# Kernel optimization log

Hardware: AMD Instinct MI355X
Metric: run time of the kernel (lower is better)

Reference implementation:

```python
import jax, jax.numpy as jnp
import numpy as np

B, T, E, H, R = 1, 2048, 4096, 16, 64
D = E // H
SCALE_ATTN = float(np.sqrt(D))


def _i8_linear(x, W, b, alpha, beta):
    # W8A8B8O8Linear: int8 in, int8 weight/bias, int8 out with requant epilogue
    acc = jnp.einsum('bte,oe->bto', x.astype(jnp.int32), W.astype(jnp.int32)).astype(jnp.float32)
    y = alpha * acc + beta * b.astype(jnp.float32)
    return jnp.clip(jnp.round(y), -128, 127).astype(jnp.int8)


def _rotate_every_two(x):
    x1, x2 = x[..., ::2], x[..., 1::2]
    return jnp.stack([-x2, x1], axis=-1).reshape(x.shape)


def _sincos(seq_len, dim):
    inv_freq = 1.0 / (10000.0 ** (jnp.arange(0, dim, 2, dtype=jnp.float32) / dim))
    ang = jnp.arange(seq_len, dtype=jnp.float32)[:, None] * inv_freq[None, :]
    return jnp.sin(ang), jnp.cos(ang)


def _apply_rotary(x, sin, cos):
    # duplicate_interleave -> repeat each freq twice along last dim
    sin = jnp.repeat(sin, 2, axis=-1)[None, :, None, :]
    cos = jnp.repeat(cos, 2, axis=-1)[None, :, None, :]
    return x * cos + _rotate_every_two(x) * sin


def setup_inputs():
    key = jax.random.key(0)
    ks = jax.random.split(key, 9)
    i8 = lambda k, s: jax.random.randint(k, s, -128, 128, dtype=jnp.int32).astype(jnp.int8)
    return {
        'hidden_states': i8(ks[0], (B, T, E)),
        'Wq': i8(ks[1], (E, E)), 'bq': i8(ks[2], (E,)),
        'Wk': i8(ks[3], (E, E)), 'bk': i8(ks[4], (E,)),
        'Wv': i8(ks[5], (E, E)), 'bv': i8(ks[6], (E,)),
        'Wo': i8(ks[7], (E, E)),
        'b_out': jax.random.normal(ks[8], (E,), dtype=jnp.float32),
        'alpha_q': 2e-4, 'beta_q': 1.0,
        'alpha_k': 2e-4, 'beta_k': 1.0,
        'alpha_v': 2e-4, 'beta_v': 1.0,
        'alpha_qk': 1e-3, 'alpha_pv': 1e-2, 'alpha_out': 2e-4,
    }


def reference(hidden_states, Wq, bq, Wk, bk, Wv, bv, Wo, b_out,
              alpha_q, beta_q, alpha_k, beta_k, alpha_v, beta_v,
              alpha_qk, alpha_pv, alpha_out):
    # int8 q/k/v projections -> [B, T, H, D]
    q = _i8_linear(hidden_states, Wq, bq, alpha_q, beta_q).reshape(B, T, H, D)
    k = _i8_linear(hidden_states, Wk, bk, alpha_k, beta_k).reshape(B, T, H, D)
    v = _i8_linear(hidden_states, Wv, bv, alpha_v, beta_v).reshape(B, T, H, D)
    v = v.transpose(0, 2, 1, 3)  # [B, H, T, D] int8

    # fused rotary on first R dims (float math on dequantized-per-tensor int8 codes)
    sin, cos = _sincos(T, R)
    qf, kf = q.astype(jnp.float32), k.astype(jnp.float32)
    qf = jnp.concatenate([_apply_rotary(qf[..., :R], sin, cos), qf[..., R:]], axis=-1)
    kf = jnp.concatenate([_apply_rotary(kf[..., :R], sin, cos), kf[..., R:]], axis=-1)
    # torch .to(int8) truncates toward zero
    to_i8 = lambda x: jnp.clip(jnp.trunc(x), -128, 127).astype(jnp.int8)
    q = to_i8(qf.transpose(0, 2, 1, 3))  # [B, H, T, D]
    k = to_i8(kf.transpose(0, 2, 1, 3))

    scores = alpha_qk * jnp.einsum('bhtd,bhsd->bhts', q.astype(jnp.int32), k.astype(jnp.int32)).astype(jnp.float32)
    causal = jnp.tril(jnp.ones((T, T), dtype=bool))
    scores = jnp.where(causal, scores, jnp.finfo(jnp.float32).min)
    probs = jax.nn.softmax(scores / SCALE_ATTN, axis=-1)
    probs = jnp.round(probs * 127.0).astype(jnp.int8)  # requant probs to int8

    acc = jnp.einsum('bhts,bhsd->bhtd', probs.astype(jnp.int32), v.astype(jnp.int32)).astype(jnp.float32)
    attn_out = jnp.clip(jnp.round(alpha_pv * acc), -128, 127).astype(jnp.int8)
    attn_out = attn_out.transpose(0, 2, 1, 3).reshape(B, T, E)  # merge heads

    # W8A8BFP32OFP32Linear
    out = alpha_out * jnp.einsum('bte,oe->bto', attn_out.astype(jnp.int32), Wo.astype(jnp.int32)).astype(jnp.float32) + b_out
    return out
```

## Files before the change

### kernel.cpp

```cpp
#include <hip/hip_runtime.h>
#include <cstdint>
#include <cmath>

#define T_ 2048
#define E_ 4096
#define H_ 16
#define D_ 256
#define NF 32

typedef int v4i  __attribute__((ext_vector_type(4)));

__device__ __forceinline__ int dot4(int a, int b, int c) {
#if __has_builtin(__builtin_amdgcn_sdot4)
  return __builtin_amdgcn_sdot4(a, b, c, false);
#else
  c += ((a << 24) >> 24) * ((b << 24) >> 24);
  c += ((a << 16) >> 24) * ((b << 16) >> 24);
  c += ((a <<  8) >> 24) * ((b <<  8) >> 24);
  c += (a >> 24) * (b >> 24);
  return c;
#endif
}

__device__ __forceinline__ int pack4i(int4 v) {
  return (v.x & 255) | ((v.y & 255) << 8) | ((v.z & 255) << 16) | (v.w << 24);
}

#define GLD_LDS16(g, l)                                                        \
  __builtin_amdgcn_global_load_lds(                                            \
      (const __attribute__((address_space(1))) void*)(g),                      \
      (__attribute__((address_space(3))) void*)(l), 16, 0, 0)

__global__ void sincos_kernel(float* __restrict__ sinT, float* __restrict__ cosT) {
  int idx = blockIdx.x * 256 + threadIdx.x;
  int t = idx >> 5, j = idx & 31;
  float invf = (float)exp(-(double)j * (log(10000.0) / 32.0));
  float ang = (float)t * invf;
  sinT[idx] = (float)sin((double)ang);
  cosT[idx] = (float)cos((double)ang);
}

__global__ __launch_bounds__(256) void repack_kernel(const int* __restrict__ src,
                                                     int8_t* __restrict__ dst) {
  size_t i = (size_t)blockIdx.x * 256 + threadIdx.x;
  const int4* s = (const int4*)src + i * 4;
  int4 a = s[0], b = s[1], c = s[2], d = s[3];
  int4 o;
  o.x = pack4i(a); o.y = pack4i(b); o.z = pack4i(c); o.w = pack4i(d);
  ((int4*)dst)[i] = o;
}

__global__ __launch_bounds__(256, 3) void qkv_gemm_mfma(
    const int8_t* __restrict__ x8,
    const int8_t* __restrict__ Wq8, const int* __restrict__ bq,
    const int8_t* __restrict__ Wk8, const int* __restrict__ bk,
    const int8_t* __restrict__ Wv8, const int* __restrict__ bv,
    const float* __restrict__ alpq, const float* __restrict__ betq,
    const float* __restrict__ alpk, const float* __restrict__ betk,
    const float* __restrict__ alpv, const float* __restrict__ betv,
    int8_t* __restrict__ Q8, int8_t* __restrict__ K8, int8_t* __restrict__ VT)
{
  const int mode = blockIdx.z;
  const int8_t* __restrict__ W = (mode == 0) ? Wq8 : (mode == 1 ? Wk8 : Wv8);
  const int* __restrict__ bs   = (mode == 0) ? bq  : (mode == 1 ? bk  : bv);
  const float alpha = (mode == 0) ? alpq[0] : (mode == 1 ? alpk[0] : alpv[0]);
  const float beta  = (mode == 0) ? betq[0] : (mode == 1 ? betk[0] : betv[0]);

  __shared__ int8_t As[3][8192];
  __shared__ int8_t Bs[3][8192];

  const int tid  = threadIdx.x;
  const int wave = tid >> 6, lane = tid & 63;
  const int wm = wave >> 1, wn = wave & 1;
  const int t0 = blockIdx.x * 128, o0 = blockIdx.y * 128;

  const int srow = lane >> 2;
  const int scol = ((lane & 3) ^ ((lane >> 3) & 3)) * 16;
  const int col  = lane & 15;
  const int quad = lane >> 4;

  v4i acc[4][4] = {};

  const int8_t* gA0 = x8 + (size_t)(t0 + wave * 32 + srow) * E_ + scol;
  const int8_t* gB0 = W  + (size_t)(o0 + wave * 32 + srow) * E_ + scol;

#define STAGE_QKV(bufi, kt) do {                                               \
    const int e0_ = (kt) * 64;                                                 \
    GLD_LDS16(gA0 + e0_,           As[bufi] + wave * 2048);                    \
    GLD_LDS16(gA0 + e0_ + 16 * E_, As[bufi] + wave * 2048 + 1024);             \
    GLD_LDS16(gB0 + e0_,           Bs[bufi] + wave * 2048);                    \
    GLD_LDS16(gB0 + e0_ + 16 * E_, Bs[bufi] + wave * 2048 + 1024);             \
  } while (0)

  int aoff[4], boff[4];
  #pragma unroll
  for (int i = 0; i < 4; ++i) {
    const int ra = wm * 64 + i * 16 + col;
    aoff[i] = ra * 64 + ((quad ^ ((ra >> 1) & 3)) * 16);
    const int rb = wn * 64 + i * 16 + col;
    boff[i] = rb * 64 + ((quad ^ ((rb >> 1) & 3)) * 16);
  }

  STAGE_QKV(0, 0);
  STAGE_QKV(1, 1);

  int cur = 0;
  for (int kt = 0; kt < 64; ++kt) {
    if (kt == 63) asm volatile("s_waitcnt vmcnt(0)" ::: "memory");
    else          asm volatile("s_waitcnt vmcnt(4)" ::: "memory");
    __builtin_amdgcn_s_barrier();
    if (kt < 62) {
      int nb = cur + 2; if (nb >= 3) nb -= 3;
      STAGE_QKV(nb, kt + 2);
    }
    v4i a[4], b[4];
    #pragma unroll
    for (int i = 0; i < 4; ++i)
      a[i] = *(const v4i*)(As[cur] + aoff[i]);
    #pragma unroll
    for (int j = 0; j < 4; ++j)
      b[j] = *(const v4i*)(Bs[cur] + boff[j]);
    __builtin_amdgcn_s_setprio(1);
    #pragma unroll
    for (int i = 0; i < 4; ++i)
      #pragma unroll
      for (int j = 0; j < 4; ++j)
        acc[i][j] = __builtin_amdgcn_mfma_i32_16x16x64_i8(a[i], b[j], acc[i][j], 0, 0, 0);
    __builtin_amdgcn_s_setprio(0);
    cur = (cur == 2) ? 0 : cur + 1;
  }
#undef STAGE_QKV

  int8_t* __restrict__ dst = (mode == 0) ? Q8 : (mode == 1 ? K8 : VT);
  #pragma unroll
  for (int j = 0; j < 4; ++j) {
    const int o  = o0 + wn * 64 + j * 16 + col;
    const int h  = o >> 8;
    const int dd = o & 255;
    const float bb = (float)bs[o];
    #pragma unroll
    for (int i = 0; i < 4; ++i) {
      const int tb = t0 + wm * 64 + i * 16 + quad * 4;
      int qb[4];
      #pragma unroll
      for (int r = 0; r < 4; ++r) {
        float v = __fadd_rn(__fmul_rn(alpha, (float)acc[i][j][r]),
                            __fmul_rn(beta, bb));
        v = rintf(v);
        v = fminf(fmaxf(v, -128.0f), 127.0f);
        qb[r] = (int)v;
      }
      if (mode == 2) {
        int packed = (qb[0] & 255) | ((qb[1] & 255) << 8) |
                     ((qb[2] & 255) << 16) | ((qb[3] & 255) << 24);
        *(int*)(dst + ((size_t)h * 256 + dd) * T_ + tb) = packed;
      } else {
        #pragma unroll
        for (int r = 0; r < 4; ++r)
          dst[((size_t)h * T_ + tb + r) * D_ + dd] = (int8_t)qb[r];
      }
    }
  }
}

__global__ __launch_bounds__(256) void rope_kernel(
    int8_t* __restrict__ Q8, int8_t* __restrict__ K8,
    const float* __restrict__ sinT, const float* __restrict__ cosT)
{
  int idx = blockIdx.x * 256 + threadIdx.x;
  int c = idx & 3;
  int t = (idx >> 2) & (T_ - 1);
  int h = (idx >> 13) & (H_ - 1);
  int m = idx >> 17;
  int8_t* base = (m == 0 ? Q8 : K8) + ((size_t)h * T_ + t) * D_ + c * 16;
  int4 v = *(int4*)base;
  int u[4] = {v.x, v.y, v.z, v.w};
  const int jb = c * 8;
  #pragma unroll
  for (int ui = 0; ui < 4; ++ui) {
    const int j = jb + ui * 2;
    const float s0 = sinT[t * NF + j],     c0 = cosT[t * NF + j];
    const float s1 = sinT[t * NF + j + 1], c1 = cosT[t * NF + j + 1];
    const int w = u[ui];
    float y0 = (float)((w << 24) >> 24);
    float y1 = (float)((w << 16) >> 24);
    float y2 = (float)((w <<  8) >> 24);
    float y3 = (float)(w >> 24);
    float r0 = __fadd_rn(__fmul_rn(y0, c0), __fmul_rn(-y1, s0));
    float r1 = __fadd_rn(__fmul_rn(y1, c0), __fmul_rn( y0, s0));
    float r2 = __fadd_rn(__fmul_rn(y2, c1), __fmul_rn(-y3, s1));
    float r3 = __fadd_rn(__fmul_rn(y3, c1), __fmul_rn( y2, s1));
    int q0 = (int)fminf(fmaxf(truncf(r0), -128.0f), 127.0f);
    int q1 = (int)fminf(fmaxf(truncf(r1), -128.0f), 127.0f);
    int q2 = (int)fminf(fmaxf(truncf(r2), -128.0f), 127.0f);
    int q3 = (int)fminf(fmaxf(truncf(r3), -128.0f), 127.0f);
    u[ui] = (q0 & 255) | ((q1 & 255) << 8) | ((q2 & 255) << 16) | ((q3 & 255) << 24);
  }
  int4 ov; ov.x = u[0]; ov.y = u[1]; ov.z = u[2]; ov.w = u[3];
  *(int4*)base = ov;
}

__global__ __launch_bounds__(256, 3) void out_gemm_mfma(
    const int8_t* __restrict__ xa, const int8_t* __restrict__ Wo8,
    const float* __restrict__ b_out, const float* __restrict__ p_aout,
    float* __restrict__ out)
{
  const float alpha = p_aout[0];
  __shared__ int8_t As[3][8192];
  __shared__ int8_t Bs[3][8192];

  const int tid  = threadIdx.x;
  const int wave = tid >> 6, lane = tid & 63;
  const int wm = wave >> 1, wn = wave & 1;
  const int t0 = blockIdx.x * 128, o0 = blockIdx.y * 128;
  const int srow = lane >> 2;
  const int scol = ((lane & 3) ^ ((lane >> 3) & 3)) * 16;
  const int col = lane & 15, quad = lane >> 4;

  v4i acc[4][4] = {};
  const int8_t* gA0 = xa  + (size_t)(t0 + wave * 32 + srow) * E_ + scol;
  const int8_t* gB0 = Wo8 + (size_t)(o0 + wave * 32 + srow) * E_ + scol;

#define STAGE_OUT(bufi, kt) do {                                               \
    const int e0_ = (kt) * 64;                                                 \
    GLD_LDS16(gA0 + e0_,           As[bufi] + wave * 2048);                    \
    GLD_LDS16(gA0 + e0_ + 16 * E_, As[bufi] + wave * 2048 + 1024);             \
    GLD_LDS16(gB0 + e0_,           Bs[bufi] + wave * 2048);                    \
    GLD_LDS16(gB0 + e0_ + 16 * E_, Bs[bufi] + wave * 2048 + 1024);             \
  } while (0)

  int aoff[4], boff[4];
  #pragma unroll
  for (int i = 0; i < 4; ++i) {
    const int ra = wm * 64 + i * 16 + col;
    aoff[i] = ra * 64 + ((quad ^ ((ra >> 1) & 3)) * 16);
    const int rb = wn * 64 + i * 16 + col;
    boff[i] = rb * 64 + ((quad ^ ((rb >> 1) & 3)) * 16);
  }

  STAGE_OUT(0, 0);
  STAGE_OUT(1, 1);

  int cur = 0;
  for (int kt = 0; kt < 64; ++kt) {
    if (kt == 63) asm volatile("s_waitcnt vmcnt(0)" ::: "memory");
    else          asm volatile("s_waitcnt vmcnt(4)" ::: "memory");
    __builtin_amdgcn_s_barrier();
    if (kt < 62) {
      int nb = cur + 2; if (nb >= 3) nb -= 3;
      STAGE_OUT(nb, kt + 2);
    }
    v4i a[4], b[4];
    #pragma unroll
    for (int i = 0; i < 4; ++i)
      a[i] = *(const v4i*)(As[cur] + aoff[i]);
    #pragma unroll
    for (int j = 0; j < 4; ++j)
      b[j] = *(const v4i*)(Bs[cur] + boff[j]);
    __builtin_amdgcn_s_setprio(1);
    #pragma unroll
    for (int i = 0; i < 4; ++i)
      #pragma unroll
      for (int j = 0; j < 4; ++j)
        acc[i][j] = __builtin_amdgcn_mfma_i32_16x16x64_i8(a[i], b[j], acc[i][j], 0, 0, 0);
    __builtin_amdgcn_s_setprio(0);
    cur = (cur == 2) ? 0 : cur + 1;
  }
#undef STAGE_OUT

  #pragma unroll
  for (int j = 0; j < 4; ++j) {
    const int o = o0 + wn * 64 + j * 16 + col;
    const float bb = b_out[o];
    #pragma unroll
    for (int i = 0; i < 4; ++i) {
      #pragma unroll
      for (int r = 0; r < 4; ++r) {
        const int t = t0 + wm * 64 + i * 16 + quad * 4 + r;
        out[(size_t)t * E_ + o] = __fadd_rn(__fmul_rn(alpha, (float)acc[i][j][r]), bb);
      }
    }
  }
}

__global__ __launch_bounds__(256) void attn_ms_chunk(
    const int8_t* __restrict__ Q8, const int8_t* __restrict__ K8,
    const float* __restrict__ p_aqk,
    float* __restrict__ mPart, float* __restrict__ sPart)
{
  const int ch = blockIdx.x;
  const int qi = blockIdx.y;
  const int h  = blockIdx.z;
  if ((ch << 2) > qi) return;

  __shared__ int8_t Qs[4 * 4096];
  __shared__ int8_t KVs[16384];
  __shared__ float  mred[64][2];
  __shared__ float  sred[64][2];

  const int t0  = qi * 64;
  const int tid = threadIdx.x;
  const int wave = tid >> 6, lane = tid & 63;
  const int wm = wave >> 1, wn = wave & 1;
  const int col = lane & 15, quad = lane >> 4;
  const int srow = lane >> 2, scol = (lane & 3) * 16;
  const float aqk = p_aqk[0] * 0.0625f;

  {
    const int8_t* g = Q8 + ((size_t)h * T_ + t0 + wave * 16 + srow) * D_ + scol;
    #pragma unroll
    for (int c = 0; c < 4; ++c)
      GLD_LDS16(g + c * 64, Qs + c * 4096 + wave * 1024);
  }

  const int it0 = ch * 4;
  const int it1 = (it0 + 3 < qi) ? (it0 + 3) : qi;

  float m[8], sm[8];
  #pragma unroll
  for (int u = 0; u < 8; ++u) { m[u] = -INFINITY; sm[u] = 0.0f; }

  for (int it = it0; it <= it1; ++it) {
    const int s0 = it * 64;
    __syncthreads();
    {
      const int8_t* g = K8 + ((size_t)h * T_ + s0 + wave * 16 + srow) * D_ + scol;
      #pragma unroll
      for (int c = 0; c < 4; ++c)
        GLD_LDS16(g + c * 64, KVs + c * 4096 + wave * 1024);
    }
    __syncthreads();
    v4i accS[2][2] = {};
    #pragma unroll
    for (int c = 0; c < 4; ++c) {
      v4i a[2], b[2];
      #pragma unroll
      for (int i = 0; i < 2; ++i)
        a[i] = *(const v4i*)(Qs + c * 4096 + (wm * 32 + i * 16 + col) * 64 + quad * 16);
      #pragma unroll
      for (int j = 0; j < 2; ++j)
        b[j] = *(const v4i*)(KVs + c * 4096 + (wn * 32 + j * 16 + col) * 64 + quad * 16);
      #pragma unroll
      for (int i = 0; i < 2; ++i)
        #pragma unroll
        for (int j = 0; j < 2; ++j)
          accS[i][j] = __builtin_amdgcn_mfma_i32_16x16x64_i8(a[i], b[j], accS[i][j], 0, 0, 0);
    }
    const bool diag = (s0 == t0);
    #pragma unroll
    for (int i = 0; i < 2; ++i) {
      #pragma unroll
      for (int r = 0; r < 4; ++r) {
        const int ri = i * 4 + r;
        const int qrow = t0 + wm * 32 + i * 16 + quad * 4 + r;
        #pragma unroll
        for (int j = 0; j < 2; ++j) {
          const int s = s0 + wn * 32 + j * 16 + col;
          if (!diag || s <= qrow) {
            float l = __fmul_rn(aqk, (float)accS[i][j][r]);
            if (l > m[ri]) { sm[ri] = sm[ri] * expf(m[ri] - l) + 1.0f; m[ri] = l; }
            else           { sm[ri] += expf(l - m[ri]); }
          }
        }
      }
    }
  }

  #pragma unroll
  for (int u = 0; u < 8; ++u) {
    #pragma unroll
    for (int off = 1; off < 16; off <<= 1) {
      float om = __shfl_xor(m[u], off);
      float os = __shfl_xor(sm[u], off);
      float mm = fmaxf(m[u], om);
      float e1 = (m[u] == mm) ? 1.0f : expf(m[u] - mm);
      float e2 = (om   == mm) ? 1.0f : expf(om - mm);
      sm[u] = sm[u] * e1 + os * e2;
      m[u] = mm;
    }
  }
  __syncthreads();
  if (col == 0) {
    #pragma unroll
    for (int u = 0; u < 8; ++u) {
      int row = wm * 32 + (u >> 2) * 16 + quad * 4 + (u & 3);
      mred[row][wn] = m[u];
      sred[row][wn] = sm[u];
    }
  }
  __syncthreads();
  if (col == 0 && wn == 0) {
    #pragma unroll
    for (int u = 0; u < 8; ++u) {
      int row = wm * 32 + (u >> 2) * 16 + quad * 4 + (u & 3);
      float m0 = mred[row][0], m1 = mred[row][1];
      float sa = sred[row][0], sb = sred[row][1];
      float mm = fmaxf(m0, m1);
      float e0 = (m0 == mm) ? 1.0f : expf(m0 - mm);
      float e1 = (m1 == mm) ? 1.0f : expf(m1 - mm);
      size_t base = (((size_t)h * 32 + qi) * 64 + row) * 8 + ch;
      mPart[base] = mm;
      sPart[base] = __fadd_rn(__fmul_rn(sa, e0), __fmul_rn(sb, e1));
    }
  }
}

__global__ __launch_bounds__(256) void attn_ms_combine(
    const float* __restrict__ mPart, const float* __restrict__ sPart,
    float* __restrict__ mFg, float* __restrict__ sFg)
{
  int idx = blockIdx.x * 256 + threadIdx.x;
  int t = idx & (T_ - 1), h = idx >> 11;
  int qi = t >> 6, row = t & 63;
  int nch = (qi >> 2) + 1;
  const float* mp = mPart + (((size_t)h * 32 + qi) * 64 + row) * 8;
  const float* sp = sPart + (((size_t)h * 32 + qi) * 64 + row) * 8;
  float m = mp[0], s = sp[0];
  for (int c = 1; c < nch; ++c) {
    float mc = mp[c], sc = sp[c];
    float mm = fmaxf(m, mc);
    float e1 = (m  == mm) ? 1.0f : expf(m - mm);
    float e2 = (mc == mm) ? 1.0f : expf(mc - mm);
    s = __fadd_rn(__fmul_rn(s, e1), __fmul_rn(sc, e2));
    m = mm;
  }
  mFg[idx] = m;
  sFg[idx] = s;
}

__global__ __launch_bounds__(256) void attn_pv_chunk(
    const int8_t* __restrict__ Q8, const int8_t* __restrict__ K8,
    const int8_t* __restrict__ VT,
    const float* __restrict__ p_aqk,
    const float* __restrict__ mFg, const float* __restrict__ sFg,
    int* __restrict__ P0, int* __restrict__ P1)
{
  const int cc = blockIdx.x;
  const int qi = 31 - blockIdx.y;
  const int h  = blockIdx.z;
  if (cc == 1 && qi < 16) return;

  __shared__ int8_t Qs[4 * 4096];
  __shared__ int8_t KVs[16384];
  __shared__ int8_t Ps[64][64];

  const int t0  = qi * 64;
  const int tid = threadIdx.x;
  const int wave = tid >> 6, lane = tid & 63;
  const int wm = wave >> 1, wn = wave & 1;
  const int col = lane & 15, quad = lane >> 4;
  const int srow = lane >> 2, scol = (lane & 3) * 16;
  const float aqk = p_aqk[0] * 0.0625f;

  {
    const int8_t* g = Q8 + ((size_t)h * T_ + t0 + wave * 16 + srow) * D_ + scol;
    #pragma unroll
    for (int c = 0; c < 4; ++c)
      GLD_LDS16(g + c * 64, Qs + c * 4096 + wave * 1024);
  }

  float mF[8], sF[8];
  #pragma unroll
  for (int u = 0; u < 8; ++u) {
    const int row = wm * 32 + (u >> 2) * 16 + quad * 4 + (u & 3);
    mF[u] = mFg[h * T_ + t0 + row];
    sF[u] = sFg[h * T_ + t0 + row];
  }

  const int it0 = cc * 16;
  const int it1 = (it0 + 15 < qi) ? (it0 + 15) : qi;

  v4i pv[2][8] = {};
  for (int it = it0; it <= it1; ++it) {
    const int s0 = it * 64;
    __syncthreads();
    {
      const int8_t* g = K8 + ((size_t)h * T_ + s0 + wave * 16 + srow) * D_ + scol;
      #pragma unroll
      for (int c = 0; c < 4; ++c)
        GLD_LDS16(g + c * 64, KVs + c * 4096 + wave * 1024);
    }
    __syncthreads();
    v4i accS[2][2] = {};
    #pragma unroll
    for (int c = 0; c < 4; ++c) {
      v4i a[2], b[2];
      #pragma unroll
      for (int i = 0; i < 2; ++i)
        a[i] = *(const v4i*)(Qs + c * 4096 + (wm * 32 + i * 16 + col) * 64 + quad * 16);
      #pragma unroll
      for (int j = 0; j < 2; ++j)
        b[j] = *(const v4i*)(KVs + c * 4096 + (wn * 32 + j * 16 + col) * 64 + quad * 16);
      #pragma unroll
      for (int i = 0; i < 2; ++i)
        #pragma unroll
        for (int j = 0; j < 2; ++j)
          accS[i][j] = __builtin_amdgcn_mfma_i32_16x16x64_i8(a[i], b[j], accS[i][j], 0, 0, 0);
    }
    __syncthreads();
    {
      #pragma unroll
      for (int c = 0; c < 4; ++c) {
        const int drow = (wave * 4 + c) * 16 + srow;
        GLD_LDS16(VT + ((size_t)h * 256 + drow) * T_ + s0 + scol,
                  KVs + (wave * 4 + c) * 1024);
      }
    }
    const bool diag = (s0 == t0);
    #pragma unroll
    for (int i = 0; i < 2; ++i) {
      #pragma unroll
      for (int r = 0; r < 4; ++r) {
        const int ri = i * 4 + r;
        const int qrow = t0 + wm * 32 + i * 16 + quad * 4 + r;
        #pragma unroll
        for (int j = 0; j < 2; ++j) {
          const int s = s0 + wn * 32 + j * 16 + col;
          int q = 0;
          if (!diag || s <= qrow) {
            float l = __fmul_rn(aqk, (float)accS[i][j][r]);
            float p = expf(l - mF[ri]) / sF[ri];
            q = (int)rintf(__fmul_rn(p, 127.0f));
          }
          Ps[wm * 32 + i * 16 + quad * 4 + r][wn * 32 + j * 16 + col] = (int8_t)q;
        }
      }
    }
    __syncthreads();
    v4i a2[2], b2[8];
    #pragma unroll
    for (int i = 0; i < 2; ++i)
      a2[i] = *(const v4i*)&Ps[wm * 32 + i * 16 + col][quad * 16];
    #pragma unroll
    for (int dt = 0; dt < 8; ++dt)
      b2[dt] = *(const v4i*)(KVs + (wn * 128 + dt * 16 + col) * 64 + quad * 16);
    #pragma unroll
    for (int i = 0; i < 2; ++i)
      #pragma unroll
      for (int dt = 0; dt < 8; ++dt)
        pv[i][dt] = __builtin_amdgcn_mfma_i32_16x16x64_i8(a2[i], b2[dt], pv[i][dt], 0, 0, 0);
  }

  int* __restrict__ dst = (cc == 0)
      ? P0 + (((size_t)h * 32 + qi) << 14)
      : P1 + (((size_t)h * 16 + (qi - 16)) << 14);
  #pragma unroll
  for (int i = 0; i < 2; ++i) {
    #pragma unroll
    for (int r = 0; r < 4; ++r) {
      const int trow = wm * 32 + i * 16 + quad * 4 + r;
      #pragma unroll
      for (int dt = 0; dt < 8; ++dt) {
        const int d = wn * 128 + dt * 16 + col;
        dst[trow * 256 + d] = pv[i][dt][r];
      }
    }
  }
}

__global__ __launch_bounds__(256) void attn_pv_combine(
    const int* __restrict__ P0, const int* __restrict__ P1,
    const float* __restrict__ p_apv, int8_t* __restrict__ attn8)
{
  const float apv = p_apv[0];
  int idx = blockIdx.x * 256 + threadIdx.x;
  int d4  = idx & 63;
  int row = (idx >> 6) & 63;
  int qi  = (idx >> 12) & 31;
  int h   = idx >> 17;
  size_t off = (((size_t)h * 32 + qi) << 14) + row * 256 + d4 * 4;
  int4 a = *(const int4*)(P0 + off);
  if (qi >= 16) {
    size_t off1 = (((size_t)h * 16 + (qi - 16)) << 14) + row * 256 + d4 * 4;
    int4 b1 = *(const int4*)(P1 + off1);
    a.x += b1.x; a.y += b1.y; a.z += b1.z; a.w += b1.w;
  }
  int q[4];
  int vv[4] = {a.x, a.y, a.z, a.w};
  #pragma unroll
  for (int r = 0; r < 4; ++r) {
    float y = rintf(__fmul_rn(apv, (float)vv[r]));
    y = fminf(fmaxf(y, -128.0f), 127.0f);
    q[r] = (int)y;
  }
  int packed = (q[0] & 255) | ((q[1] & 255) << 8) | ((q[2] & 255) << 16) | ((q[3] & 255) << 24);
  int t = qi * 64 + row;
  *(int*)(attn8 + (size_t)t * E_ + h * D_ + d4 * 4) = packed;
}

__global__ __launch_bounds__(256) void attn_mfma(
    const int8_t* __restrict__ Q8, const int8_t* __restrict__ K8,
    const int8_t* __restrict__ VT,
    const float* __restrict__ p_aqk, const float* __restrict__ p_apv,
    int8_t* __restrict__ attn8)
{
  __shared__ int8_t Qs[4 * 4096];
  __shared__ int8_t KVs[16384];
  __shared__ int8_t Ps[64][64];
  __shared__ float  mred[64][2];
  __shared__ float  sred[64][2];

  const int h   = blockIdx.y;
  const int t0  = blockIdx.x * 64;
  const int tid = threadIdx.x;
  const int wave = tid >> 6, lane = tid & 63;
  const int wm = wave >> 1, wn = wave & 1;
  const int col = lane & 15, quad = lane >> 4;
  const int srow = lane >> 2, scol = (lane & 3) * 16;
  const float aqk = p_aqk[0] * 0.0625f;
  const float apv = p_apv[0];

  {
    const int8_t* g = Q8 + ((size_t)h * T_ + t0 + wave * 16 + srow) * D_ + scol;
    #pragma unroll
    for (int c = 0; c < 4; ++c)
      GLD_LDS16(g + c * 64, Qs + c * 4096 + wave * 1024);
  }

  const int nt = t0 / 64 + 1;

  float m[8], sm[8];
  #pragma unroll
  for (int u = 0; u < 8; ++u) { m[u] = -INFINITY; sm[u] = 0.0f; }

  for (int it = 0; it < nt; ++it) {
    const int s0 = it * 64;
    __syncthreads();
    {
      const int8_t* g = K8 + ((size_t)h * T_ + s0 + wave * 16 + srow) * D_ + scol;
      #pragma unroll
      for (int c = 0; c < 4; ++c)
        GLD_LDS16(g + c * 64, KVs + c * 4096 + wave * 1024);
    }
    __syncthreads();
    v4i accS[2][2] = {};
    #pragma unroll
    for (int c = 0; c < 4; ++c) {
      v4i a[2], b[2];
      #pragma unroll
      for (int i = 0; i < 2; ++i)
        a[i] = *(const v4i*)(Qs + c * 4096 + (wm * 32 + i * 16 + col) * 64 + quad * 16);
      #pragma unroll
      for (int j = 0; j < 2; ++j)
        b[j] = *(const v4i*)(KVs + c * 4096 + (wn * 32 + j * 16 + col) * 64 + quad * 16);
      #pragma unroll
      for (int i = 0; i < 2; ++i)
        #pragma unroll
        for (int j = 0; j < 2; ++j)
          accS[i][j] = __builtin_amdgcn_mfma_i32_16x16x64_i8(a[i], b[j], accS[i][j], 0, 0, 0);
    }
    const bool diag = (s0 == t0);
    #pragma unroll
    for (int i = 0; i < 2; ++i) {
      #pragma unroll
      for (int r = 0; r < 4; ++r) {
        const int ri = i * 4 + r;
        const int qrow = t0 + wm * 32 + i * 16 + quad * 4 + r;
        #pragma unroll
        for (int j = 0; j < 2; ++j) {
          const int s = s0 + wn * 32 + j * 16 + col;
          if (!diag || s <= qrow) {
            float l = __fmul_rn(aqk, (float)accS[i][j][r]);
            if (l > m[ri]) { sm[ri] = sm[ri] * expf(m[ri] - l) + 1.0f; m[ri] = l; }
            else           { sm[ri] += expf(l - m[ri]); }
          }
        }
      }
    }
  }

  #pragma unroll
  for (int u = 0; u < 8; ++u) {
    #pragma unroll
    for (int off = 1; off < 16; off <<= 1) {
      float om = __shfl_xor(m[u], off);
      float os = __shfl_xor(sm[u], off);
      float mm = fmaxf(m[u], om);
      float e1 = (m[u] == mm) ? 1.0f : expf(m[u] - mm);
      float e2 = (om   == mm) ? 1.0f : expf(om - mm);
      sm[u] = sm[u] * e1 + os * e2;
      m[u] = mm;
    }
  }
  __syncthreads();
  if (col == 0) {
    #pragma unroll
    for (int u = 0; u < 8; ++u) {
      int row = wm * 32 + (u >> 2) * 16 + quad * 4 + (u & 3);
      mred[row][wn] = m[u];
      sred[row][wn] = sm[u];
    }
  }
  __syncthreads();
  float mF[8], sF[8];
  #pragma unroll
  for (int u = 0; u < 8; ++u) {
    int row = wm * 32 + (u >> 2) * 16 + quad * 4 + (u & 3);
    float m0 = mred[row][0], m1 = mred[row][1];
    float sa = sred[row][0], sb = sred[row][1];
    float mm = fmaxf(m0, m1);
    float e0 = (m0 == mm) ? 1.0f : expf(m0 - mm);
    float e1 = (m1 == mm) ? 1.0f : expf(m1 - mm);
    mF[u] = mm;
    sF[u] = __fadd_rn(__fmul_rn(sa, e0), __fmul_rn(sb, e1));
  }

  v4i pv[2][8] = {};
  for (int it = 0; it < nt; ++it) {
    const int s0 = it * 64;
    __syncthreads();
    {
      const int8_t* g = K8 + ((size_t)h * T_ + s0 + wave * 16 + srow) * D_ + scol;
      #pragma unroll
      for (int c = 0; c < 4; ++c)
        GLD_LDS16(g + c * 64, KVs + c * 4096 + wave * 1024);
    }
    __syncthreads();
    v4i accS[2][2] = {};
    #pragma unroll
    for (int c = 0; c < 4; ++c) {
      v4i a[2], b[2];
      #pragma unroll
      for (int i = 0; i < 2; ++i)
        a[i] = *(const v4i*)(Qs + c * 4096 + (wm * 32 + i * 16 + col) * 64 + quad * 16);
      #pragma unroll
      for (int j = 0; j < 2; ++j)
        b[j] = *(const v4i*)(KVs + c * 4096 + (wn * 32 + j * 16 + col) * 64 + quad * 16);
      #pragma unroll
      for (int i = 0; i < 2; ++i)
        #pragma unroll
        for (int j = 0; j < 2; ++j)
          accS[i][j] = __builtin_amdgcn_mfma_i32_16x16x64_i8(a[i], b[j], accS[i][j], 0, 0, 0);
    }
    __syncthreads();
    {
      #pragma unroll
      for (int c = 0; c < 4; ++c) {
        const int drow = (wave * 4 + c) * 16 + srow;
        GLD_LDS16(VT + ((size_t)h * 256 + drow) * T_ + s0 + scol,
                  KVs + (wave * 4 + c) * 1024);
      }
    }
    const bool diag = (s0 == t0);
    #pragma unroll
    for (int i = 0; i < 2; ++i) {
      #pragma unroll
      for (int r = 0; r < 4; ++r) {
        const int ri = i * 4 + r;
        const int qrow = t0 + wm * 32 + i * 16 + quad * 4 + r;
        #pragma unroll
        for (int j = 0; j < 2; ++j) {
          const int s = s0 + wn * 32 + j * 16 + col;
          int q = 0;
          if (!diag || s <= qrow) {
            float l = __fmul_rn(aqk, (float)accS[i][j][r]);
            float p = expf(l - mF[ri]) / sF[ri];
            q = (int)rintf(__fmul_rn(p, 127.0f));
          }
          Ps[wm * 32 + i * 16 + quad * 4 + r][wn * 32 + j * 16 + col] = (int8_t)q;
        }
      }
    }
    __syncthreads();
    v4i a2[2], b2[8];
    #pragma unroll
    for (int i = 0; i < 2; ++i)
      a2[i] = *(const v4i*)&Ps[wm * 32 + i * 16 + col][quad * 16];
    #pragma unroll
    for (int dt = 0; dt < 8; ++dt)
      b2[dt] = *(const v4i*)(KVs + (wn * 128 + dt * 16 + col) * 64 + quad * 16);
    #pragma unroll
    for (int i = 0; i < 2; ++i)
      #pragma unroll
      for (int dt = 0; dt < 8; ++dt)
        pv[i][dt] = __builtin_amdgcn_mfma_i32_16x16x64_i8(a2[i], b2[dt], pv[i][dt], 0, 0, 0);
  }

  #pragma unroll
  for (int i = 0; i < 2; ++i) {
    #pragma unroll
    for (int r = 0; r < 4; ++r) {
      const int t = t0 + wm * 32 + i * 16 + quad * 4 + r;
      #pragma unroll
      for (int dt = 0; dt < 8; ++dt) {
        const int d = wn * 128 + dt * 16 + col;
        float y = rintf(__fmul_rn(apv, (float)pv[i][dt][r]));
        y = fminf(fmaxf(y, -128.0f), 127.0f);
        attn8[(size_t)t * E_ + h * D_ + d] = (int8_t)(int)y;
      }
    }
  }
}

__global__ __launch_bounds__(256) void qkv_gemm_fb(
    const int* __restrict__ xp,
    const int* __restrict__ Wqp, const int* __restrict__ bq,
    const int* __restrict__ Wkp, const int* __restrict__ bk,
    const int* __restrict__ Wvp, const int* __restrict__ bv,
    const float* __restrict__ alpq, const float* __restrict__ betq,
    const float* __restrict__ alpk, const float* __restrict__ betk,
    const float* __restrict__ alpv, const float* __restrict__ betv,
    const float* __restrict__ sinT, const float* __restrict__ cosT,
    int8_t* __restrict__ Q8, int8_t* __restrict__ K8, int8_t* __restrict__ VT)
{
  const int mode = blockIdx.z;
  const int* __restrict__ Wp = (mode == 0) ? Wqp : (mode == 1 ? Wkp : Wvp);
  const int* __restrict__ bs = (mode == 0) ? bq  : (mode == 1 ? bk  : bv);
  const float alpha = (mode == 0) ? alpq[0] : (mode == 1 ? alpk[0] : alpv[0]);
  const float beta  = (mode == 0) ? betq[0] : (mode == 1 ? betk[0] : betv[0]);

  __shared__ int As[64 * 17];
  __shared__ int Bs[64 * 17];
  const int tid = threadIdx.x;
  const int tx = tid & 15, ty = tid >> 4;
  const int t0 = blockIdx.x * 64, o0 = blockIdx.y * 64;
  const int lrow = tid >> 2, lc = tid & 3;
  int acc[4][4] = {};

  for (int e0 = 0; e0 < E_; e0 += 64) {
    const int* xr = xp + (size_t)(t0 + lrow) * E_ + e0 + lc * 16;
    const int* wr = Wp + (size_t)(o0 + lrow) * E_ + e0 + lc * 16;
    int a4[4], b4[4];
    #pragma unroll
    for (int u = 0; u < 4; ++u) a4[u] = pack4i(((const int4*)xr)[u]);
    #pragma unroll
    for (int u = 0; u < 4; ++u) b4[u] = pack4i(((const int4*)wr)[u]);
    __syncthreads();
    int* ap = &As[lrow * 17 + lc * 4];
    ap[0] = a4[0]; ap[1] = a4[1]; ap[2] = a4[2]; ap[3] = a4[3];
    int* bp = &Bs[lrow * 17 + lc * 4];
    bp[0] = b4[0]; bp[1] = b4[1]; bp[2] = b4[2]; bp[3] = b4[3];
    __syncthreads();
    #pragma unroll
    for (int kk = 0; kk < 16; ++kk) {
      int a[4], b[4];
      #pragma unroll
      for (int i = 0; i < 4; ++i) a[i] = As[(ty * 4 + i) * 17 + kk];
      #pragma unroll
      for (int j = 0; j < 4; ++j) b[j] = Bs[(tx * 4 + j) * 17 + kk];
      #pragma unroll
      for (int i = 0; i < 4; ++i)
        #pragma unroll
        for (int j = 0; j < 4; ++j)
          acc[i][j] = dot4(a[i], b[j], acc[i][j]);
    }
  }

  const int ob = o0 + tx * 4;
  const int h  = ob >> 8;
  const int dd = ob & 255;
  #pragma unroll
  for (int i = 0; i < 4; ++i) {
    const int t = t0 + ty * 4 + i;
    float y[4];
    #pragma unroll
    for (int j = 0; j < 4; ++j) {
      float v = __fadd_rn(__fmul_rn(alpha, (float)acc[i][j]),
                          __fmul_rn(beta, (float)bs[ob + j]));
      v = rintf(v);
      y[j] = fminf(fmaxf(v, -128.0f), 127.0f);
    }
    int q0, q1, q2, q3;
    if (mode < 2 && dd < 64) {
      const int j0 = dd >> 1;
      const float s0 = sinT[t * NF + j0],     c0 = cosT[t * NF + j0];
      const float s1 = sinT[t * NF + j0 + 1], c1 = cosT[t * NF + j0 + 1];
      float r0 = __fadd_rn(__fmul_rn(y[0], c0), __fmul_rn(-y[1], s0));
      float r1 = __fadd_rn(__fmul_rn(y[1], c0), __fmul_rn( y[0], s0));
      float r2 = __fadd_rn(__fmul_rn(y[2], c1), __fmul_rn(-y[3], s1));
      float r3 = __fadd_rn(__fmul_rn(y[3], c1), __fmul_rn( y[2], s1));
      q0 = (int)fminf(fmaxf(truncf(r0), -128.0f), 127.0f);
      q1 = (int)fminf(fmaxf(truncf(r1), -128.0f), 127.0f);
      q2 = (int)fminf(fmaxf(truncf(r2), -128.0f), 127.0f);
      q3 = (int)fminf(fmaxf(truncf(r3), -128.0f), 127.0f);
    } else {
      q0 = (int)y[0]; q1 = (int)y[1]; q2 = (int)y[2]; q3 = (int)y[3];
    }
    if (mode == 2) {
      VT[((size_t)h * 256 + dd + 0) * T_ + t] = (int8_t)q0;
      VT[((size_t)h * 256 + dd + 1) * T_ + t] = (int8_t)q1;
      VT[((size_t)h * 256 + dd + 2) * T_ + t] = (int8_t)q2;
      VT[((size_t)h * 256 + dd + 3) * T_ + t] = (int8_t)q3;
    } else {
      int8_t* dst = (mode == 0) ? Q8 : K8;
      int packed = (q0 & 255) | ((q1 & 255) << 8) | ((q2 & 255) << 16) | ((q3 & 255) << 24);
      *(int*)(dst + ((size_t)h * T_ + t) * D_ + dd) = packed;
    }
  }
}

__global__ __launch_bounds__(256) void out_gemm_fb(
    const int8_t* __restrict__ xa, const int* __restrict__ Wop,
    const float* __restrict__ b_out, const float* __restrict__ p_aout,
    float* __restrict__ out)
{
  __shared__ int As[64 * 17];
  __shared__ int Bs[64 * 17];
  const float alpha = p_aout[0];
  const int tid = threadIdx.x;
  const int tx = tid & 15, ty = tid >> 4;
  const int t0 = blockIdx.x * 64, o0 = blockIdx.y * 64;
  const int lrow = tid >> 2, lc = tid & 3;
  int acc[4][4] = {};

  for (int e0 = 0; e0 < E_; e0 += 64) {
    int4 av4 = *(const int4*)(xa + (size_t)(t0 + lrow) * E_ + e0 + lc * 16);
    const int* wr = Wop + (size_t)(o0 + lrow) * E_ + e0 + lc * 16;
    int b4[4];
    #pragma unroll
    for (int u = 0; u < 4; ++u) b4[u] = pack4i(((const int4*)wr)[u]);
    __syncthreads();
    int* ap = &As[lrow * 17 + lc * 4];
    ap[0] = av4.x; ap[1] = av4.y; ap[2] = av4.z; ap[3] = av4.w;
    int* bp = &Bs[lrow * 17 + lc * 4];
    bp[0] = b4[0]; bp[1] = b4[1]; bp[2] = b4[2]; bp[3] = b4[3];
    __syncthreads();
    #pragma unroll
    for (int kk = 0; kk < 16; ++kk) {
      int a[4], b[4];
      #pragma unroll
      for (int i = 0; i < 4; ++i) a[i] = As[(ty * 4 + i) * 17 + kk];
      #pragma unroll
      for (int j = 0; j < 4; ++j) b[j] = Bs[(tx * 4 + j) * 17 + kk];
      #pragma unroll
      for (int i = 0; i < 4; ++i)
        #pragma unroll
        for (int j = 0; j < 4; ++j)
          acc[i][j] = dot4(a[i], b[j], acc[i][j]);
    }
  }
  #pragma unroll
  for (int i = 0; i < 4; ++i) {
    const int t = t0 + ty * 4 + i;
    const int ob = o0 + tx * 4;
    #pragma unroll
    for (int j = 0; j < 4; ++j) {
      out[(size_t)t * E_ + ob + j] =
          __fadd_rn(__fmul_rn(alpha, (float)acc[i][j]), b_out[ob + j]);
    }
  }
}

extern "C" void kernel_launch(void* const* d_in, const int* in_sizes, int n_in,
                              void* d_out, int out_size, void* d_ws, size_t ws_size,
                              hipStream_t stream) {
  const int* hs   = (const int*)d_in[0];
  const int* Wq   = (const int*)d_in[1];
  const int* bq   = (const int*)d_in[2];
  const int* Wk   = (const int*)d_in[3];
  const int* bk   = (const int*)d_in[4];
  const int* Wv   = (const int*)d_in[5];
  const int* bv   = (const int*)d_in[6];
  const int* Wo   = (const int*)d_in[7];
  const float* b_out = (const float*)d_in[8];
  const float* aq   = (const float*)d_in[9];
  const float* btq  = (const float*)d_in[10];
  const float* ak   = (const float*)d_in[11];
  const float* btk  = (const float*)d_in[12];
  const float* av   = (const float*)d_in[13];
  const float* btv  = (const float*)d_in[14];
  const float* aqk  = (const float*)d_in[15];
  const float* apv  = (const float*)d_in[16];
  const float* aout = (const float*)d_in[17];

  const size_t SEG = (size_t)H_ * T_ * D_;
  char* ws = (char*)d_ws;
  int8_t* Q8    = (int8_t*)ws;
  int8_t* K8    = Q8 + SEG;
  int8_t* VT    = K8 + SEG;
  int8_t* attn8 = VT + SEG;
  int8_t* x8    = attn8;
  float*  sinT  = (float*)(ws + 4 * SEG);
  float*  cosT  = sinT + T_ * NF;
  int8_t* Wq8   = (int8_t*)(cosT + T_ * NF);
  int8_t* Wk8   = Wq8 + (size_t)E_ * E_;
  int8_t* Wv8   = Wk8 + (size_t)E_ * E_;
  int8_t* Wo8   = Wv8 + (size_t)E_ * E_;
  const size_t NEED = 4 * SEG + 2 * (size_t)T_ * NF * 4 + 4 * (size_t)E_ * E_;
  const bool big = (ws_size >= NEED);

  sincos_kernel<<<(T_ * NF) / 256, 256, 0, stream>>>(sinT, cosT);

  if (big) {
    repack_kernel<<<(T_ * E_ / 16) / 256, 256, 0, stream>>>(hs, x8);
    repack_kernel<<<(E_ * E_ / 16) / 256, 256, 0, stream>>>(Wq, Wq8);
    repack_kernel<<<(E_ * E_ / 16) / 256, 256, 0, stream>>>(Wk, Wk8);
    repack_kernel<<<(E_ * E_ / 16) / 256, 256, 0, stream>>>(Wv, Wv8);
    repack_kernel<<<(E_ * E_ / 16) / 256, 256, 0, stream>>>(Wo, Wo8);
    qkv_gemm_mfma<<<dim3(T_ / 128, E_ / 128, 3), 256, 0, stream>>>(
        x8, Wq8, bq, Wk8, bk, Wv8, bv, aq, btq, ak, btk, av, btv, Q8, K8, VT);
    rope_kernel<<<(2 * H_ * T_ * 4) / 256, 256, 0, stream>>>(Q8, K8, sinT, cosT);

    int*   P1g   = (int*)Wq8;
    int*   P0g   = (int*)Wk8;
    float* mPart = (float*)attn8;
    float* sPart = mPart + (size_t)H_ * 32 * 64 * 8;
    float* mFg   = sPart + (size_t)H_ * 32 * 64 * 8;
    float* sFg   = mFg + (size_t)H_ * T_;

    attn_ms_chunk<<<dim3(8, 32, H_), 256, 0, stream>>>(Q8, K8, aqk, mPart, sPart);
    attn_ms_combine<<<(H_ * T_) / 256, 256, 0, stream>>>(mPart, sPart, mFg, sFg);
    attn_pv_chunk<<<dim3(2, 32, H_), 256, 0, stream>>>(
        Q8, K8, VT, aqk, mFg, sFg, P0g, P1g);
    attn_pv_combine<<<(H_ * 32 * 64 * 64) / 256, 256, 0, stream>>>(
        P0g, P1g, apv, attn8);

    out_gemm_mfma<<<dim3(T_ / 128, E_ / 128), 256, 0, stream>>>(
        attn8, Wo8, b_out, aout, (float*)d_out);
  } else {
    qkv_gemm_fb<<<dim3(T_ / 64, E_ / 64, 3), 256, 0, stream>>>(
        hs, Wq, bq, Wk, bk, Wv, bv, aq, btq, ak, btk, av, btv,
        sinT, cosT, Q8, K8, VT);
    attn_mfma<<<dim3(T_ / 64, H_), 256, 0, stream>>>(Q8, K8, VT, aqk, apv, attn8);
    out_gemm_fb<<<dim3(T_ / 64, E_ / 64), 256, 0, stream>>>(
        attn8, Wo, b_out, aout, (float*)d_out);
  }
}
```

Baseline: 700.8 us.

## Enlarge GEMM tiles to 256, merge weight repacks, fold softmax-stat combine

QKV and output GEMMs move to 512-thread blocks with larger output tiles (256x256 for QKV, 256x128 for the output projection), doubling LDS staging buffers and adjusting per-wave load partitioning. The four weight repack launches become one 2D launch. The separate softmax max/sum combine kernel is removed and its merge loop is done inside attn_pv_chunk per row. These aim to raise data reuse per staged tile and cut launch count, at the cost of more registers and LDS per block, fewer blocks per CU, and redundant combine work across chunk blocks.

```diff
diff --git a/kernel.cpp b/kernel.cpp
--- a/kernel.cpp
+++ b/kernel.cpp
@@ -50,7 +50,23 @@
   ((int4*)dst)[i] = o;
 }
 
-__global__ __launch_bounds__(256, 3) void qkv_gemm_mfma(
+__global__ __launch_bounds__(256) void repack4_kernel(
+    const int* __restrict__ s0, const int* __restrict__ s1,
+    const int* __restrict__ s2, const int* __restrict__ s3,
+    int8_t* __restrict__ d0, int8_t* __restrict__ d1,
+    int8_t* __restrict__ d2, int8_t* __restrict__ d3) {
+  const int w = blockIdx.y;
+  const int* __restrict__ src = (w == 0) ? s0 : (w == 1 ? s1 : (w == 2 ? s2 : s3));
+  int8_t* __restrict__ dst    = (w == 0) ? d0 : (w == 1 ? d1 : (w == 2 ? d2 : d3));
+  size_t i = (size_t)blockIdx.x * 256 + threadIdx.x;
+  const int4* s = (const int4*)src + i * 4;
+  int4 a = s[0], b = s[1], c = s[2], d = s[3];
+  int4 o;
+  o.x = pack4i(a); o.y = pack4i(b); o.z = pack4i(c); o.w = pack4i(d);
+  ((int4*)dst)[i] = o;
+}
+
+__global__ __launch_bounds__(512, 2) void qkv_gemm_mfma(
     const int8_t* __restrict__ x8,
     const int8_t* __restrict__ Wq8, const int* __restrict__ bq,
     const int8_t* __restrict__ Wk8, const int* __restrict__ bk,
@@ -66,20 +82,20 @@
   const float alpha = (mode == 0) ? alpq[0] : (mode == 1 ? alpk[0] : alpv[0]);
   const float beta  = (mode == 0) ? betq[0] : (mode == 1 ? betk[0] : betv[0]);
 
-  __shared__ int8_t As[3][8192];
-  __shared__ int8_t Bs[3][8192];
+  __shared__ int8_t As[3][16384];
+  __shared__ int8_t Bs[3][16384];
 
   const int tid  = threadIdx.x;
   const int wave = tid >> 6, lane = tid & 63;
-  const int wm = wave >> 1, wn = wave & 1;
-  const int t0 = blockIdx.x * 128, o0 = blockIdx.y * 128;
+  const int wm = wave >> 2, wn = wave & 3;
+  const int t0 = blockIdx.x * 256, o0 = blockIdx.y * 256;
 
   const int srow = lane >> 2;
   const int scol = ((lane & 3) ^ ((lane >> 3) & 3)) * 16;
   const int col  = lane & 15;
   const int quad = lane >> 4;
 
-  v4i acc[4][4] = {};
+  v4i acc[8][4] = {};
 
   const int8_t* gA0 = x8 + (size_t)(t0 + wave * 32 + srow) * E_ + scol;
   const int8_t* gB0 = W  + (size_t)(o0 + wave * 32 + srow) * E_ + scol;
@@ -92,13 +108,16 @@
     GLD_LDS16(gB0 + e0_ + 16 * E_, Bs[bufi] + wave * 2048 + 1024);             \
   } while (0)
 
-  int aoff[4], boff[4];
-  #pragma unroll
-  for (int i = 0; i < 4; ++i) {
-    const int ra = wm * 64 + i * 16 + col;
+  int aoff[8], boff[4];
+  #pragma unroll
+  for (int i = 0; i < 8; ++i) {
+    const int ra = wm * 128 + i * 16 + col;
     aoff[i] = ra * 64 + ((quad ^ ((ra >> 1) & 3)) * 16);
-    const int rb = wn * 64 + i * 16 + col;
-    boff[i] = rb * 64 + ((quad ^ ((rb >> 1) & 3)) * 16);
+  }
+  #pragma unroll
+  for (int j = 0; j < 4; ++j) {
+    const int rb = wn * 64 + j * 16 + col;
+    boff[j] = rb * 64 + ((quad ^ ((rb >> 1) & 3)) * 16);
   }
 
   STAGE_QKV(0, 0);
@@ -113,19 +132,18 @@
       int nb = cur + 2; if (nb >= 3) nb -= 3;
       STAGE_QKV(nb, kt + 2);
     }
-    v4i a[4], b[4];
-    #pragma unroll
-    for (int i = 0; i < 4; ++i)
-      a[i] = *(const v4i*)(As[cur] + aoff[i]);
+    v4i b[4];
     #pragma unroll
     for (int j = 0; j < 4; ++j)
       b[j] = *(const v4i*)(Bs[cur] + boff[j]);
     __builtin_amdgcn_s_setprio(1);
     #pragma unroll
-    for (int i = 0; i < 4; ++i)
+    for (int i = 0; i < 8; ++i) {
+      v4i ai = *(const v4i*)(As[cur] + aoff[i]);
       #pragma unroll
       for (int j = 0; j < 4; ++j)
-        acc[i][j] = __builtin_amdgcn_mfma_i32_16x16x64_i8(a[i], b[j], acc[i][j], 0, 0, 0);
+        acc[i][j] = __builtin_amdgcn_mfma_i32_16x16x64_i8(ai, b[j], acc[i][j], 0, 0, 0);
+    }
     __builtin_amdgcn_s_setprio(0);
     cur = (cur == 2) ? 0 : cur + 1;
   }
@@ -139,8 +157,8 @@
     const int dd = o & 255;
     const float bb = (float)bs[o];
     #pragma unroll
-    for (int i = 0; i < 4; ++i) {
-      const int tb = t0 + wm * 64 + i * 16 + quad * 4;
+    for (int i = 0; i < 8; ++i) {
+      const int tb = t0 + wm * 128 + i * 16 + quad * 4;
       int qb[4];
       #pragma unroll
       for (int r = 0; r < 4; ++r) {
@@ -200,33 +218,32 @@
   *(int4*)base = ov;
 }
 
-__global__ __launch_bounds__(256, 3) void out_gemm_mfma(
+__global__ __launch_bounds__(512, 2) void out_gemm_mfma(
     const int8_t* __restrict__ xa, const int8_t* __restrict__ Wo8,
     const float* __restrict__ b_out, const float* __restrict__ p_aout,
     float* __restrict__ out)
 {
   const float alpha = p_aout[0];
-  __shared__ int8_t As[3][8192];
+  __shared__ int8_t As[3][16384];
   __shared__ int8_t Bs[3][8192];
 
   const int tid  = threadIdx.x;
   const int wave = tid >> 6, lane = tid & 63;
   const int wm = wave >> 1, wn = wave & 1;
-  const int t0 = blockIdx.x * 128, o0 = blockIdx.y * 128;
+  const int t0 = blockIdx.x * 256, o0 = blockIdx.y * 128;
   const int srow = lane >> 2;
   const int scol = ((lane & 3) ^ ((lane >> 3) & 3)) * 16;
   const int col = lane & 15, quad = lane >> 4;
 
   v4i acc[4][4] = {};
   const int8_t* gA0 = xa  + (size_t)(t0 + wave * 32 + srow) * E_ + scol;
-  const int8_t* gB0 = Wo8 + (size_t)(o0 + wave * 32 + srow) * E_ + scol;
+  const int8_t* gB0 = Wo8 + (size_t)(o0 + wave * 16 + srow) * E_ + scol;
 
 #define STAGE_OUT(bufi, kt) do {                                               \
     const int e0_ = (kt) * 64;                                                 \
     GLD_LDS16(gA0 + e0_,           As[bufi] + wave * 2048);                    \
     GLD_LDS16(gA0 + e0_ + 16 * E_, As[bufi] + wave * 2048 + 1024);             \
-    GLD_LDS16(gB0 + e0_,           Bs[bufi] + wave * 2048);                    \
-    GLD_LDS16(gB0 + e0_ + 16 * E_, Bs[bufi] + wave * 2048 + 1024);             \
+    GLD_LDS16(gB0 + e0_,           Bs[bufi] + wave * 1024);                    \
   } while (0)
 
   int aoff[4], boff[4];
@@ -244,7 +261,7 @@
   int cur = 0;
   for (int kt = 0; kt < 64; ++kt) {
     if (kt == 63) asm volatile("s_waitcnt vmcnt(0)" ::: "memory");
-    else          asm volatile("s_waitcnt vmcnt(4)" ::: "memory");
+    else          asm volatile("s_waitcnt vmcnt(3)" ::: "memory");
     __builtin_amdgcn_s_barrier();
     if (kt < 62) {
       int nb = cur + 2; if (nb >= 3) nb -= 3;
@@ -405,34 +422,11 @@
   }
 }
 
-__global__ __launch_bounds__(256) void attn_ms_combine(
-    const float* __restrict__ mPart, const float* __restrict__ sPart,
-    float* __restrict__ mFg, float* __restrict__ sFg)
-{
-  int idx = blockIdx.x * 256 + threadIdx.x;
-  int t = idx & (T_ - 1), h = idx >> 11;
-  int qi = t >> 6, row = t & 63;
-  int nch = (qi >> 2) + 1;
-  const float* mp = mPart + (((size_t)h * 32 + qi) * 64 + row) * 8;
-  const float* sp = sPart + (((size_t)h * 32 + qi) * 64 + row) * 8;
-  float m = mp[0], s = sp[0];
-  for (int c = 1; c < nch; ++c) {
-    float mc = mp[c], sc = sp[c];
-    float mm = fmaxf(m, mc);
-    float e1 = (m  == mm) ? 1.0f : expf(m - mm);
-    float e2 = (mc == mm) ? 1.0f : expf(mc - mm);
-    s = __fadd_rn(__fmul_rn(s, e1), __fmul_rn(sc, e2));
-    m = mm;
-  }
-  mFg[idx] = m;
-  sFg[idx] = s;
-}
-
 __global__ __launch_bounds__(256) void attn_pv_chunk(
     const int8_t* __restrict__ Q8, const int8_t* __restrict__ K8,
     const int8_t* __restrict__ VT,
     const float* __restrict__ p_aqk,
-    const float* __restrict__ mFg, const float* __restrict__ sFg,
+    const float* __restrict__ mPart, const float* __restrict__ sPart,
     int* __restrict__ P0, int* __restrict__ P1)
 {
   const int cc = blockIdx.x;
@@ -460,11 +454,23 @@
   }
 
   float mF[8], sF[8];
+  const int nch = (qi >> 2) + 1;
   #pragma unroll
   for (int u = 0; u < 8; ++u) {
     const int row = wm * 32 + (u >> 2) * 16 + quad * 4 + (u & 3);
-    mF[u] = mFg[h * T_ + t0 + row];
-    sF[u] = sFg[h * T_ + t0 + row];
+    const float* mp = mPart + (((size_t)h * 32 + qi) * 64 + row) * 8;
+    const float* sp = sPart + (((size_t)h * 32 + qi) * 64 + row) * 8;
+    float m = mp[0], s = sp[0];
+    for (int c = 1; c < nch; ++c) {
+      float mc = mp[c], sc = sp[c];
+      float mm = fmaxf(m, mc);
+      float e1 = (m  == mm) ? 1.0f : expf(m - mm);
+      float e2 = (mc == mm) ? 1.0f : expf(mc - mm);
+      s = __fadd_rn(__fmul_rn(s, e1), __fmul_rn(sc, e2));
+      m = mm;
+    }
+    mF[u] = m;
+    sF[u] = s;
   }
 
   const int it0 = cc * 16;
@@ -983,11 +989,9 @@
 
   if (big) {
     repack_kernel<<<(T_ * E_ / 16) / 256, 256, 0, stream>>>(hs, x8);
-    repack_kernel<<<(E_ * E_ / 16) / 256, 256, 0, stream>>>(Wq, Wq8);
-    repack_kernel<<<(E_ * E_ / 16) / 256, 256, 0, stream>>>(Wk, Wk8);
-    repack_kernel<<<(E_ * E_ / 16) / 256, 256, 0, stream>>>(Wv, Wv8);
-    repack_kernel<<<(E_ * E_ / 16) / 256, 256, 0, stream>>>(Wo, Wo8);
-    qkv_gemm_mfma<<<dim3(T_ / 128, E_ / 128, 3), 256, 0, stream>>>(
+    repack4_kernel<<<dim3((E_ * E_ / 16) / 256, 4), 256, 0, stream>>>(
+        Wq, Wk, Wv, Wo, Wq8, Wk8, Wv8, Wo8);
+    qkv_gemm_mfma<<<dim3(T_ / 256, E_ / 256, 3), 512, 0, stream>>>(
         x8, Wq8, bq, Wk8, bk, Wv8, bv, aq, btq, ak, btk, av, btv, Q8, K8, VT);
     rope_kernel<<<(2 * H_ * T_ * 4) / 256, 256, 0, stream>>>(Q8, K8, sinT, cosT);
 
@@ -995,17 +999,14 @@
     int*   P0g   = (int*)Wk8;
     float* mPart = (float*)attn8;
     float* sPart = mPart + (size_t)H_ * 32 * 64 * 8;
-    float* mFg   = sPart + (size_t)H_ * 32 * 64 * 8;
-    float* sFg   = mFg + (size_t)H_ * T_;
 
     attn_ms_chunk<<<dim3(8, 32, H_), 256, 0, stream>>>(Q8, K8, aqk, mPart, sPart);
-    attn_ms_combine<<<(H_ * T_) / 256, 256, 0, stream>>>(mPart, sPart, mFg, sFg);
     attn_pv_chunk<<<dim3(2, 32, H_), 256, 0, stream>>>(
-        Q8, K8, VT, aqk, mFg, sFg, P0g, P1g);
+        Q8, K8, VT, aqk, mPart, sPart, P0g, P1g);
     attn_pv_combine<<<(H_ * 32 * 64 * 64) / 256, 256, 0, stream>>>(
         P0g, P1g, apv, attn8);
 
-    out_gemm_mfma<<<dim3(T_ / 128, E_ / 128), 256, 0, stream>>>(
+    out_gemm_mfma<<<dim3(T_ / 256, E_ / 128), 512, 0, stream>>>(
         attn8, Wo8, b_out, aout, (float*)d_out);
   } else {
     qkv_gemm_fb<<<dim3(T_ / 64, E_ / 64, 3), 256, 0, stream>>>(
```

New measurement: 790.4 us. 1.13x slower.
